# Kernel optimization log

Measured on AMD Instinct MI355X. Metric: run time of the kernel, lower is better.

## Reference

```python
import jax, jax.numpy as jnp
import numpy as np


def _make_kernels():
    k3 = jnp.array([[0, 1, 0], [1, -4, 1], [0, 1, 0]], dtype=jnp.float32)
    k3 = jnp.tile(k3[None, None], (4, 1, 1, 1))  # [4,1,3,3] depthwise OIHW
    k5 = jnp.array([[0, 0, -1, 0, 0],
                    [0, -1, -2, -1, 0],
                    [-1, -2, 16, -2, -1],
                    [0, -1, -2, -1, 0],
                    [0, 0, -1, 0, 0]], dtype=jnp.float32)
    k5 = jnp.tile(k5[None, None], (4, 1, 1, 1))  # [4,1,5,5]
    return k3, k5


def setup_inputs() -> dict:
    key = jax.random.key(0)
    x = jax.random.normal(key, (32, 4, 512, 512), dtype=jnp.float32)
    k3, k5 = _make_kernels()
    return {"x": x, "k3": k3, "k5": k5}


def _dwconv(x, k, pad):
    # depthwise conv: groups == in_channels == 4
    return jax.lax.conv_general_dilated(
        x, k,
        window_strides=(1, 1),
        padding=((pad, pad), (pad, pad)),
        dimension_numbers=("NCHW", "OIHW", "NCHW"),
        feature_group_count=4,
    )


def reference(x, k3, k5):
    e3 = _dwconv(x, k3, 1)                 # [B,4,H,W]
    e5 = _dwconv(x, k5, 2)                 # [B,4,H,W]
    response = jnp.maximum(jnp.abs(e3), jnp.abs(e5))
    edge_map = jnp.max(response, axis=1, keepdims=True)  # [B,1,H,W]
    v_min = jnp.min(edge_map, axis=(1, 2, 3), keepdims=True)
    v_max = jnp.max(edge_map, axis=(1, 2, 3), keepdims=True)
    return (edge_map - v_min) / (v_max - v_min + 1e-6)
```

## Files before the change

### kernel.cpp

```cpp
#include <hip/hip_runtime.h>

#define IH 512
#define IW 512
#define NC 4
#define NB 32
#define RPT 4
#define NTILES 2048

typedef float v4f __attribute__((ext_vector_type(4)));

__device__ __forceinline__ void load_row8(const float* __restrict__ xc, int hh,
                                          int w, bool v0, bool v2,
                                          float* __restrict__ dst) {
    if (hh < 0 || hh >= IH) {
        #pragma unroll
        for (int j = 0; j < 8; ++j) dst[j] = 0.f;
        return;
    }
    const float* rowp = xc + (size_t)hh * IW + w;
    float2 a  = v0 ? *(const float2*)(rowp - 2) : float2{0.f, 0.f};
    float4 bb =      *(const float4*)(rowp);
    float2 cc = v2 ? *(const float2*)(rowp + 4) : float2{0.f, 0.f};
    dst[0] = a.x;  dst[1] = a.y;
    dst[2] = bb.x; dst[3] = bb.y; dst[4] = bb.z; dst[5] = bb.w;
    dst[6] = cc.x; dst[7] = cc.y;
}

__global__ __launch_bounds__(256, 4) void edge_kernel(
        const float* __restrict__ x, float* __restrict__ out,
        float* __restrict__ slotmin, float* __restrict__ slotmax) {
    const int qx    = threadIdx.x & 31;
    const int ty    = threadIdx.x >> 5;
    const int w     = blockIdx.x * 128 + qx * 4;
    const int hbase = blockIdx.y * (8 * RPT) + ty * RPT;
    const int b     = blockIdx.z;

    const bool v0 = (w >= 4);
    const bool v2 = (w <= IW - 8);

    float resp[RPT][4];
    #pragma unroll
    for (int k = 0; k < RPT; ++k)
        #pragma unroll
        for (int j = 0; j < 4; ++j) resp[k][j] = 0.f;

    const float* xb = x + (size_t)b * NC * IH * IW;

    #pragma unroll 1
    for (int c = 0; c < NC; ++c) {
        const float* xc = xb + (size_t)c * IH * IW;

        float r[RPT + 4][8];
        #pragma unroll
        for (int rr = 0; rr < RPT + 4; ++rr)
            load_row8(xc, hbase - 2 + rr, w, v0, v2, r[rr]);

        #pragma unroll
        for (int k = 0; k < RPT; ++k) {
            const float* rm2 = r[k + 0];
            const float* rm1 = r[k + 1];
            const float* r0c = r[k + 2];
            const float* rp1 = r[k + 3];
            const float* rp2 = r[k + 4];

            #pragma unroll
            for (int j = 0; j < 4; ++j) {
                const int i = 2 + j;
                const float c0     = r0c[i];
                const float cross1 = rm1[i] + rp1[i] + r0c[i - 1] + r0c[i + 1];
                const float e3     = cross1 - 4.f * c0;
                const float ring   = rm2[i] + rp2[i] + r0c[i - 2] + r0c[i + 2]
                                   + rm1[i - 1] + rm1[i + 1]
                                   + rp1[i - 1] + rp1[i + 1];
                const float e5     = 16.f * c0 - 2.f * cross1 - ring;
                const float rc     = fmaxf(fabsf(e3), fabsf(e5));
                resp[k][j] = fmaxf(resp[k][j], rc);
            }
        }
    }

    float* ob = out + ((size_t)b * IH + hbase) * IW + w;
    #pragma unroll
    for (int k = 0; k < RPT; ++k) {
        float4 o;
        o.x = resp[k][0]; o.y = resp[k][1]; o.z = resp[k][2]; o.w = resp[k][3];
        *(float4*)(ob + (size_t)k * IW) = o;
    }

    float lmin = resp[0][0], lmax = resp[0][0];
    #pragma unroll
    for (int k = 0; k < RPT; ++k)
        #pragma unroll
        for (int j = 0; j < 4; ++j) {
            lmin = fminf(lmin, resp[k][j]);
            lmax = fmaxf(lmax, resp[k][j]);
        }
    #pragma unroll
    for (int off = 32; off >= 1; off >>= 1) {
        lmin = fminf(lmin, __shfl_down(lmin, off));
        lmax = fmaxf(lmax, __shfl_down(lmax, off));
    }
    __shared__ float smin[4], smax[4];
    const int wave = threadIdx.x >> 6;
    const int lane = threadIdx.x & 63;
    if (lane == 0) { smin[wave] = lmin; smax[wave] = lmax; }
    __syncthreads();
    if (threadIdx.x == 0) {
        const float m0 = fminf(fminf(smin[0], smin[1]), fminf(smin[2], smin[3]));
        const float M0 = fmaxf(fmaxf(smax[0], smax[1]), fmaxf(smax[2], smax[3]));
        const int slot = b * 64 + blockIdx.y * 4 + blockIdx.x;
        slotmin[slot] = m0;
        slotmax[slot] = M0;
    }
}

__global__ __launch_bounds__(256) void norm_tile(
        float* __restrict__ out,
        const float* __restrict__ slotmin,
        const float* __restrict__ slotmax) {
    const int qx    = threadIdx.x & 31;
    const int tyg   = threadIdx.x >> 5;
    const int w     = blockIdx.x * 128 + qx * 4;
    const int hbase = blockIdx.y * (8 * RPT) + tyg * RPT;
    const int b     = blockIdx.z;

    __shared__ float sv[2];
    if (threadIdx.x < 64) {
        float mn = slotmin[b * 64 + threadIdx.x];
        float mx = slotmax[b * 64 + threadIdx.x];
        #pragma unroll
        for (int off = 32; off >= 1; off >>= 1) {
            mn = fminf(mn, __shfl_down(mn, off));
            mx = fmaxf(mx, __shfl_down(mx, off));
        }
        if (threadIdx.x == 0) { sv[0] = mn; sv[1] = mx; }
    }
    __syncthreads();
    const float vmin = sv[0];
    const float inv  = 1.0f / (sv[1] - vmin + 1e-6f);

    float* ob = out + ((size_t)b * IH + hbase) * IW + w;
    #pragma unroll
    for (int k = 0; k < RPT; ++k) {
        const float4 u = *(const float4*)(ob + (size_t)k * IW);
        v4f o;
        o.x = (u.x - vmin) * inv;
        o.y = (u.y - vmin) * inv;
        o.z = (u.z - vmin) * inv;
        o.w = (u.w - vmin) * inv;
        __builtin_nontemporal_store(o, (v4f*)(ob + (size_t)k * IW));
    }
}

extern "C" void kernel_launch(void* const* d_in, const int* in_sizes, int n_in,
                              void* d_out, int out_size, void* d_ws, size_t ws_size,
                              hipStream_t stream) {
    const float* x = (const float*)d_in[0];
    float* out = (float*)d_out;
    float* slotmin = (float*)d_ws;
    float* slotmax = slotmin + NTILES;

    hipLaunchKernelGGL(edge_kernel, dim3(4, 16, NB), dim3(256), 0, stream,
                       x, out, slotmin, slotmax);
    hipLaunchKernelGGL(norm_tile, dim3(4, 16, NB), dim3(256), 0, stream,
                       out, slotmin, slotmax);
}
```

Baseline: 216.5 us.

## Fuse edge and normalize kernels via persistent blocks and atomic grid barrier

Replaces the two-kernel scheme with a single persistent kernel of 512 blocks. Each block computes four tiles, keeps the responses in registers, publishes per-tile min/max and bumps a per-image atomic counter. It then spins until all 64 tiles of each of its images are done and writes normalized output directly. This removes the unnormalized write and read-back of the output and one kernel launch, at the cost of more registers per thread and a spin-wait that assumes all 512 blocks are co-resident.

Measured after the change: 324.9 us. +50.0%, slower.

```diff
diff --git a/kernel.cpp b/kernel.cpp
--- a/kernel.cpp
+++ b/kernel.cpp
@@ -6,8 +6,14 @@
 #define NB 32
 #define RPT 4
 #define NTILES 2048
+#define NBLK2 512
+#define TPB 4
 
 typedef float v4f __attribute__((ext_vector_type(4)));
+
+__global__ void init_cnt(unsigned int* __restrict__ cnt) {
+    if (threadIdx.x < NB) cnt[threadIdx.x] = 0u;
+}
 
 __device__ __forceinline__ void load_row8(const float* __restrict__ xc, int hh,
                                           int w, bool v0, bool v2,
@@ -26,19 +32,18 @@
     dst[6] = cc.x; dst[7] = cc.y;
 }
 
-__global__ __launch_bounds__(256, 4) void edge_kernel(
-        const float* __restrict__ x, float* __restrict__ out,
-        float* __restrict__ slotmin, float* __restrict__ slotmax) {
-    const int qx    = threadIdx.x & 31;
-    const int ty    = threadIdx.x >> 5;
-    const int w     = blockIdx.x * 128 + qx * 4;
-    const int hbase = blockIdx.y * (8 * RPT) + ty * RPT;
-    const int b     = blockIdx.z;
+__device__ __forceinline__ void compute_tile(const float* __restrict__ x,
+                                             int t, int qx, int tyg,
+                                             float (&resp)[RPT][4]) {
+    const int tx    = t & 3;
+    const int ty    = (t >> 2) & 15;
+    const int b     = t >> 6;
+    const int w     = tx * 128 + qx * 4;
+    const int hbase = ty * (8 * RPT) + tyg * RPT;
 
     const bool v0 = (w >= 4);
     const bool v2 = (w <= IW - 8);
 
-    float resp[RPT][4];
     #pragma unroll
     for (int k = 0; k < RPT; ++k)
         #pragma unroll
@@ -78,77 +83,101 @@
             }
         }
     }
+}
 
-    float* ob = out + ((size_t)b * IH + hbase) * IW + w;
+__global__ __launch_bounds__(256, 2) void edge_fused(
+        const float* __restrict__ x, float* __restrict__ out,
+        float* __restrict__ slotmin, float* __restrict__ slotmax,
+        unsigned int* __restrict__ cnt) {
+    const int qx  = threadIdx.x & 31;
+    const int tyg = threadIdx.x >> 5;
+    const int B   = blockIdx.x;
+
+    __shared__ float smin[4], smax[4];
+    __shared__ float snorm[TPB][2];
+
+    float resp[TPB][RPT][4];
+
     #pragma unroll
-    for (int k = 0; k < RPT; ++k) {
-        float4 o;
-        o.x = resp[k][0]; o.y = resp[k][1]; o.z = resp[k][2]; o.w = resp[k][3];
-        *(float4*)(ob + (size_t)k * IW) = o;
+    for (int s = 0; s < TPB; ++s) {
+        const int t = B + s * NBLK2;
+        compute_tile(x, t, qx, tyg, resp[s]);
+
+        float lmin = resp[s][0][0], lmax = resp[s][0][0];
+        #pragma unroll
+        for (int k = 0; k < RPT; ++k)
+            #pragma unroll
+            for (int j = 0; j < 4; ++j) {
+                lmin = fminf(lmin, resp[s][k][j]);
+                lmax = fmaxf(lmax, resp[s][k][j]);
+            }
+        #pragma unroll
+        for (int off = 32; off >= 1; off >>= 1) {
+            lmin = fminf(lmin, __shfl_down(lmin, off));
+            lmax = fmaxf(lmax, __shfl_down(lmax, off));
+        }
+        const int wave = threadIdx.x >> 6;
+        const int lane = threadIdx.x & 63;
+        if (lane == 0) { smin[wave] = lmin; smax[wave] = lmax; }
+        __syncthreads();
+        if (threadIdx.x == 0) {
+            const float m0 = fminf(fminf(smin[0], smin[1]),
+                                   fminf(smin[2], smin[3]));
+            const float M0 = fmaxf(fmaxf(smax[0], smax[1]),
+                                   fmaxf(smax[2], smax[3]));
+            __hip_atomic_store(&slotmin[t], m0, __ATOMIC_RELAXED,
+                               __HIP_MEMORY_SCOPE_AGENT);
+            __hip_atomic_store(&slotmax[t], M0, __ATOMIC_RELAXED,
+                               __HIP_MEMORY_SCOPE_AGENT);
+            __hip_atomic_fetch_add(&cnt[t >> 6], 1u, __ATOMIC_RELEASE,
+                                   __HIP_MEMORY_SCOPE_AGENT);
+        }
+        __syncthreads();
     }
 
-    float lmin = resp[0][0], lmax = resp[0][0];
-    #pragma unroll
-    for (int k = 0; k < RPT; ++k)
-        #pragma unroll
-        for (int j = 0; j < 4; ++j) {
-            lmin = fminf(lmin, resp[k][j]);
-            lmax = fmaxf(lmax, resp[k][j]);
-        }
+    const int wv = threadIdx.x >> 6;
+    const int ln = threadIdx.x & 63;
+    const int img = (B >> 6) + 8 * wv;
+    if (ln == 0) {
+        while (__hip_atomic_load(&cnt[img], __ATOMIC_ACQUIRE,
+                                 __HIP_MEMORY_SCOPE_AGENT) < 64u)
+            __builtin_amdgcn_s_sleep(2);
+    }
+    float mn = __hip_atomic_load(&slotmin[img * 64 + ln], __ATOMIC_RELAXED,
+                                 __HIP_MEMORY_SCOPE_AGENT);
+    float mx = __hip_atomic_load(&slotmax[img * 64 + ln], __ATOMIC_RELAXED,
+                                 __HIP_MEMORY_SCOPE_AGENT);
     #pragma unroll
     for (int off = 32; off >= 1; off >>= 1) {
-        lmin = fminf(lmin, __shfl_down(lmin, off));
-        lmax = fmaxf(lmax, __shfl_down(lmax, off));
+        mn = fminf(mn, __shfl_down(mn, off));
+        mx = fmaxf(mx, __shfl_down(mx, off));
     }
-    __shared__ float smin[4], smax[4];
-    const int wave = threadIdx.x >> 6;
-    const int lane = threadIdx.x & 63;
-    if (lane == 0) { smin[wave] = lmin; smax[wave] = lmax; }
-    __syncthreads();
-    if (threadIdx.x == 0) {
-        const float m0 = fminf(fminf(smin[0], smin[1]), fminf(smin[2], smin[3]));
-        const float M0 = fmaxf(fmaxf(smax[0], smax[1]), fmaxf(smax[2], smax[3]));
-        const int slot = b * 64 + blockIdx.y * 4 + blockIdx.x;
-        slotmin[slot] = m0;
-        slotmax[slot] = M0;
-    }
-}
-
-__global__ __launch_bounds__(256) void norm_tile(
-        float* __restrict__ out,
-        const float* __restrict__ slotmin,
-        const float* __restrict__ slotmax) {
-    const int qx    = threadIdx.x & 31;
-    const int tyg   = threadIdx.x >> 5;
-    const int w     = blockIdx.x * 128 + qx * 4;
-    const int hbase = blockIdx.y * (8 * RPT) + tyg * RPT;
-    const int b     = blockIdx.z;
-
-    __shared__ float sv[2];
-    if (threadIdx.x < 64) {
-        float mn = slotmin[b * 64 + threadIdx.x];
-        float mx = slotmax[b * 64 + threadIdx.x];
-        #pragma unroll
-        for (int off = 32; off >= 1; off >>= 1) {
-            mn = fminf(mn, __shfl_down(mn, off));
-            mx = fmaxf(mx, __shfl_down(mx, off));
-        }
-        if (threadIdx.x == 0) { sv[0] = mn; sv[1] = mx; }
+    if (ln == 0) {
+        snorm[wv][0] = mn;
+        snorm[wv][1] = 1.0f / (mx - mn + 1e-6f);
     }
     __syncthreads();
-    const float vmin = sv[0];
-    const float inv  = 1.0f / (sv[1] - vmin + 1e-6f);
 
-    float* ob = out + ((size_t)b * IH + hbase) * IW + w;
     #pragma unroll
-    for (int k = 0; k < RPT; ++k) {
-        const float4 u = *(const float4*)(ob + (size_t)k * IW);
-        v4f o;
-        o.x = (u.x - vmin) * inv;
-        o.y = (u.y - vmin) * inv;
-        o.z = (u.z - vmin) * inv;
-        o.w = (u.w - vmin) * inv;
-        __builtin_nontemporal_store(o, (v4f*)(ob + (size_t)k * IW));
+    for (int s = 0; s < TPB; ++s) {
+        const int t     = B + s * NBLK2;
+        const float vmn = snorm[s][0];
+        const float inv = snorm[s][1];
+        const int tx    = t & 3;
+        const int ty    = (t >> 2) & 15;
+        const int b     = t >> 6;
+        const int w     = tx * 128 + qx * 4;
+        const int hbase = ty * (8 * RPT) + tyg * RPT;
+        float* ob = out + ((size_t)b * IH + hbase) * IW + w;
+        #pragma unroll
+        for (int k = 0; k < RPT; ++k) {
+            v4f o;
+            o.x = (resp[s][k][0] - vmn) * inv;
+            o.y = (resp[s][k][1] - vmn) * inv;
+            o.z = (resp[s][k][2] - vmn) * inv;
+            o.w = (resp[s][k][3] - vmn) * inv;
+            __builtin_nontemporal_store(o, (v4f*)(ob + (size_t)k * IW));
+        }
     }
 }
 
@@ -159,9 +188,9 @@
     float* out = (float*)d_out;
     float* slotmin = (float*)d_ws;
     float* slotmax = slotmin + NTILES;
+    unsigned int* cnt = (unsigned int*)(slotmax + NTILES);
 
-    hipLaunchKernelGGL(edge_kernel, dim3(4, 16, NB), dim3(256), 0, stream,
-                       x, out, slotmin, slotmax);
-    hipLaunchKernelGGL(norm_tile, dim3(4, 16, NB), dim3(256), 0, stream,
-                       out, slotmin, slotmax);
+    hipLaunchKernelGGL(init_cnt, dim3(1), dim3(64), 0, stream, cnt);
+    hipLaunchKernelGGL(edge_fused, dim3(NBLK2), dim3(256), 0, stream,
+                       x, out, slotmin, slotmax, cnt);
 }
```

## Stage input tiles into LDS via global_load_lds for stencil reuse

Applied to the files above, without the earlier changes.

The per-thread global loads of an 8-row halo window are replaced by cooperative staging of each 36x140 channel tile into shared memory using direct global-to-LDS loads, with out-of-bounds chunks pointing at a zero page. Threads then read their stencil windows from LDS with a rotating 5-row register buffer. This is meant to cut redundant global/L2 traffic from overlapping halos and the many small unaligned loads. In exchange it adds two block barriers per channel with no overlap between staging and compute, plus LDS usage that may limit occupancy.

Result: no change. 214.3 us (-1.0%).

```diff
diff --git a/kernel.cpp b/kernel.cpp
--- a/kernel.cpp
+++ b/kernel.cpp
@@ -6,37 +6,83 @@
 #define NB 32
 #define RPT 4
 #define NTILES 2048
+#define TW 140
+#define TROWS 36
+#define CPR 35
+#define NCHUNK (CPR * TROWS)
 
 typedef float v4f __attribute__((ext_vector_type(4)));
 
-__device__ __forceinline__ void load_row8(const float* __restrict__ xc, int hh,
-                                          int w, bool v0, bool v2,
-                                          float* __restrict__ dst) {
-    if (hh < 0 || hh >= IH) {
-        #pragma unroll
-        for (int j = 0; j < 8; ++j) dst[j] = 0.f;
-        return;
-    }
-    const float* rowp = xc + (size_t)hh * IW + w;
-    float2 a  = v0 ? *(const float2*)(rowp - 2) : float2{0.f, 0.f};
-    float4 bb =      *(const float4*)(rowp);
-    float2 cc = v2 ? *(const float2*)(rowp + 4) : float2{0.f, 0.f};
-    dst[0] = a.x;  dst[1] = a.y;
-    dst[2] = bb.x; dst[3] = bb.y; dst[4] = bb.z; dst[5] = bb.w;
-    dst[6] = cc.x; dst[7] = cc.y;
-}
-
-__global__ __launch_bounds__(256, 4) void edge_kernel(
+__device__ __attribute__((aligned(16))) const float ZEROPAGE[4] = {0.f, 0.f, 0.f, 0.f};
+
+typedef const __attribute__((address_space(1))) void gvoid_t;
+typedef __attribute__((address_space(3))) void svoid_t;
+
+__device__ __forceinline__ void stage_tile(const float* __restrict__ xc,
+                                           float* __restrict__ lbuf,
+                                           int R0, int C0, int wv, int ln) {
+    const int bases[5] = {0, 256, 512, 768, NCHUNK - 256};
+    #pragma unroll
+    for (int rno = 0; rno < 5; ++rno) {
+        const int chunk = bases[rno] + wv * 64 + ln;
+        const int row   = chunk / CPR;
+        const int blk   = chunk - row * CPR;
+        const int gr    = R0 - 2 + row;
+        const int gc    = C0 - 4 + blk * 4;
+        const bool valid = (gr >= 0) & (gr < IH) & (gc >= 0) & (gc + 4 <= IW);
+        const float* src = valid ? (xc + (size_t)gr * IW + gc) : ZEROPAGE;
+        float* ldst = lbuf + (size_t)(bases[rno] + wv * 64) * 4;
+        __builtin_amdgcn_global_load_lds((gvoid_t*)src, (svoid_t*)ldst, 16, 0, 0);
+    }
+}
+
+__device__ __forceinline__ void load_wrow(const float* __restrict__ lds,
+                                          int Lr, int qx, float* __restrict__ d) {
+    const float* p = lds + Lr * TW + qx * 4 + 2;
+    float2 a  = *(const float2*)(p + 0);
+    float2 b  = *(const float2*)(p + 2);
+    float2 c  = *(const float2*)(p + 4);
+    float2 dd = *(const float2*)(p + 6);
+    d[0] = a.x;  d[1] = a.y;  d[2] = b.x;  d[3] = b.y;
+    d[4] = c.x;  d[5] = c.y;  d[6] = dd.x; d[7] = dd.y;
+}
+
+__device__ __forceinline__ void stencil_row(const float* __restrict__ rm2,
+                                            const float* __restrict__ rm1,
+                                            const float* __restrict__ r0c,
+                                            const float* __restrict__ rp1,
+                                            const float* __restrict__ rp2,
+                                            float* __restrict__ acc) {
+    #pragma unroll
+    for (int j = 0; j < 4; ++j) {
+        const int i = 2 + j;
+        const float c0     = r0c[i];
+        const float cross1 = rm1[i] + rp1[i] + r0c[i - 1] + r0c[i + 1];
+        const float e3     = cross1 - 4.f * c0;
+        const float ring   = rm2[i] + rp2[i] + r0c[i - 2] + r0c[i + 2]
+                           + rm1[i - 1] + rm1[i + 1]
+                           + rp1[i - 1] + rp1[i + 1];
+        const float e5     = 16.f * c0 - 2.f * cross1 - ring;
+        const float rc     = fmaxf(fabsf(e3), fabsf(e5));
+        acc[j] = fmaxf(acc[j], rc);
+    }
+}
+
+__global__ __launch_bounds__(256, 4) void edge_tiled(
         const float* __restrict__ x, float* __restrict__ out,
         float* __restrict__ slotmin, float* __restrict__ slotmax) {
-    const int qx    = threadIdx.x & 31;
-    const int ty    = threadIdx.x >> 5;
-    const int w     = blockIdx.x * 128 + qx * 4;
-    const int hbase = blockIdx.y * (8 * RPT) + ty * RPT;
-    const int b     = blockIdx.z;
-
-    const bool v0 = (w >= 4);
-    const bool v2 = (w <= IW - 8);
+    __shared__ float lds[NCHUNK * 4];
+    __shared__ float smin[4], smax[4];
+
+    const int qx  = threadIdx.x & 31;
+    const int tyg = (threadIdx.x >> 5) & 7;
+    const int wv  = threadIdx.x >> 6;
+    const int ln  = threadIdx.x & 63;
+    const int C0  = blockIdx.x * 128;
+    const int R0  = blockIdx.y * 32;
+    const int b   = blockIdx.z;
+
+    const float* xb = x + (size_t)b * NC * IH * IW;
 
     float resp[RPT][4];
     #pragma unroll
@@ -44,41 +90,31 @@
         #pragma unroll
         for (int j = 0; j < 4; ++j) resp[k][j] = 0.f;
 
-    const float* xb = x + (size_t)b * NC * IH * IW;
-
     #pragma unroll 1
     for (int c = 0; c < NC; ++c) {
-        const float* xc = xb + (size_t)c * IH * IW;
-
-        float r[RPT + 4][8];
-        #pragma unroll
-        for (int rr = 0; rr < RPT + 4; ++rr)
-            load_row8(xc, hbase - 2 + rr, w, v0, v2, r[rr]);
-
-        #pragma unroll
-        for (int k = 0; k < RPT; ++k) {
-            const float* rm2 = r[k + 0];
-            const float* rm1 = r[k + 1];
-            const float* r0c = r[k + 2];
-            const float* rp1 = r[k + 3];
-            const float* rp2 = r[k + 4];
-
-            #pragma unroll
-            for (int j = 0; j < 4; ++j) {
-                const int i = 2 + j;
-                const float c0     = r0c[i];
-                const float cross1 = rm1[i] + rp1[i] + r0c[i - 1] + r0c[i + 1];
-                const float e3     = cross1 - 4.f * c0;
-                const float ring   = rm2[i] + rp2[i] + r0c[i - 2] + r0c[i + 2]
-                                   + rm1[i - 1] + rm1[i + 1]
-                                   + rp1[i - 1] + rp1[i + 1];
-                const float e5     = 16.f * c0 - 2.f * cross1 - ring;
-                const float rc     = fmaxf(fabsf(e3), fabsf(e5));
-                resp[k][j] = fmaxf(resp[k][j], rc);
-            }
-        }
-    }
-
+        stage_tile(xb + (size_t)c * IH * IW, lds, R0, C0, wv, ln);
+        __syncthreads();
+
+        const int r0 = tyg * 4;
+        float w0[8], w1[8], w2[8], w3[8], w4[8];
+        load_wrow(lds, r0 + 0, qx, w0);
+        load_wrow(lds, r0 + 1, qx, w1);
+        load_wrow(lds, r0 + 2, qx, w2);
+        load_wrow(lds, r0 + 3, qx, w3);
+        load_wrow(lds, r0 + 4, qx, w4);
+        stencil_row(w0, w1, w2, w3, w4, resp[0]);
+        load_wrow(lds, r0 + 5, qx, w0);
+        stencil_row(w1, w2, w3, w4, w0, resp[1]);
+        load_wrow(lds, r0 + 6, qx, w1);
+        stencil_row(w2, w3, w4, w0, w1, resp[2]);
+        load_wrow(lds, r0 + 7, qx, w2);
+        stencil_row(w3, w4, w0, w1, w2, resp[3]);
+
+        __syncthreads();
+    }
+
+    const int w     = C0 + qx * 4;
+    const int hbase = R0 + tyg * 4;
     float* ob = out + ((size_t)b * IH + hbase) * IW + w;
     #pragma unroll
     for (int k = 0; k < RPT; ++k) {
@@ -100,10 +136,7 @@
         lmin = fminf(lmin, __shfl_down(lmin, off));
         lmax = fmaxf(lmax, __shfl_down(lmax, off));
     }
-    __shared__ float smin[4], smax[4];
-    const int wave = threadIdx.x >> 6;
-    const int lane = threadIdx.x & 63;
-    if (lane == 0) { smin[wave] = lmin; smax[wave] = lmax; }
+    if (ln == 0) { smin[wv] = lmin; smax[wv] = lmax; }
     __syncthreads();
     if (threadIdx.x == 0) {
         const float m0 = fminf(fminf(smin[0], smin[1]), fminf(smin[2], smin[3]));
@@ -160,7 +193,7 @@
     float* slotmin = (float*)d_ws;
     float* slotmax = slotmin + NTILES;
 
-    hipLaunchKernelGGL(edge_kernel, dim3(4, 16, NB), dim3(256), 0, stream,
+    hipLaunchKernelGGL(edge_tiled, dim3(4, 16, NB), dim3(256), 0, stream,
                        x, out, slotmin, slotmax);
     hipLaunchKernelGGL(norm_tile, dim3(4, 16, NB), dim3(256), 0, stream,
                        out, slotmin, slotmax);
```
